# Kernel tuning notes

Hardware: AMD Instinct MI355X
Metric: run time of the kernel (lower is better)

Reference implementation:

```python
import jax, jax.numpy as jnp
import numpy as np

B, S, D, U = 32, 2048, 1024, 1024


def setup_inputs() -> dict:
    key = jax.random.key(0)
    ks = jax.random.split(key, 8)
    scale_in = 1.0 / np.sqrt(D)
    scale_u = 1.0 / np.sqrt(U)
    return {
        "query": jax.random.normal(ks[0], (B, D), dtype=jnp.float32),
        "values": jax.random.normal(ks[1], (B, S, D), dtype=jnp.float32),
        "W1": jax.random.normal(ks[2], (D, U), dtype=jnp.float32) * scale_in,
        "b1": jnp.zeros((U,), dtype=jnp.float32),
        "W2": jax.random.normal(ks[3], (D, U), dtype=jnp.float32) * scale_in,
        "b2": jnp.zeros((U,), dtype=jnp.float32),
        "V": jax.random.normal(ks[4], (U, 1), dtype=jnp.float32) * scale_u,
        "bV": jnp.zeros((1,), dtype=jnp.float32),
    }


def reference(query, values, W1, b1, W2, b2, V, bV):
    # values: [B, S, D] -> [B, S, U]; query: [B, D] -> [B, 1, U]
    proj_v = jnp.einsum("bsd,du->bsu", values, W1) + b1
    proj_q = (query @ W2 + b2)[:, None, :]
    # score: [B, S, 1]
    score = jnp.einsum("bsu,uo->bso", jnp.tanh(proj_v + proj_q), V) + bV
    attention_weights = jax.nn.softmax(score, axis=1)
    # context: [B, D]
    context_vector = jnp.sum(attention_weights * values, axis=1)
    return (context_vector, attention_weights)
```

## Files before the change

### kernel.cpp

```cpp
#include <hip/hip_runtime.h>

#define DEVFN __device__ __forceinline__

typedef __attribute__((ext_vector_type(4))) float f32x4;
typedef __attribute__((ext_vector_type(8))) short short8;
typedef __attribute__((ext_vector_type(4))) unsigned int uint4v;
typedef __attribute__((ext_vector_type(8))) unsigned short ushort8;

constexpr int CB = 32;
constexpr int CS = 2048;
constexpr int CD = 1024;
constexpr int CU = 1024;
constexpr int CM = CB * CS;

DEVFN unsigned f2bf_u(float f) {
    unsigned u = __float_as_uint(f);
    return (u + 0x7FFFu + ((u >> 16) & 1u)) >> 16;
}
DEVFN unsigned f2bf_pack(float lo, float hi) {
    return f2bf_u(lo) | (f2bf_u(hi) << 16);
}
DEVFN short8 cvt8(f32x4 a, f32x4 b) {
    uint4v p;
    p[0] = f2bf_pack(a[0], a[1]);
    p[1] = f2bf_pack(a[2], a[3]);
    p[2] = f2bf_pack(b[0], b[1]);
    p[3] = f2bf_pack(b[2], b[3]);
    return __builtin_bit_cast(short8, p);
}
DEVFN float tanh_fast(float x) {
    float e = exp2f(x * 2.885390081777927f);
    return 1.0f - 2.0f * __builtin_amdgcn_rcpf(e + 1.0f);
}

__global__ void k_bias1(const float* __restrict__ q, const float* __restrict__ W2,
                        float* __restrict__ bpart) {
    int dc = blockIdx.x, b = blockIdx.y;
    int t = threadIdx.x;
    __shared__ float qs[128];
    if (t < 128) qs[t] = q[b * CD + dc * 128 + t];
    __syncthreads();
    float acc0 = 0.f, acc1 = 0.f, acc2 = 0.f, acc3 = 0.f;
    const float* w2 = W2 + (size_t)(dc * 128) * CU + t;
#pragma unroll 4
    for (int d = 0; d < 128; ++d) {
        float qv = qs[d];
        const float* r = w2 + (size_t)d * CU;
        acc0 += qv * r[0];
        acc1 += qv * r[256];
        acc2 += qv * r[512];
        acc3 += qv * r[768];
    }
    float* o = bpart + (size_t)(b * 8 + dc) * CU + t;
    o[0] = acc0; o[256] = acc1; o[512] = acc2; o[768] = acc3;
}

__global__ void k_bias2(const float* __restrict__ bpart, const float* __restrict__ b1,
                        const float* __restrict__ b2, float* __restrict__ bias) {
    int idx = blockIdx.x * 256 + threadIdx.x;
    int b = idx >> 10, u = idx & 1023;
    float s = b1[u] + b2[u];
#pragma unroll
    for (int dc = 0; dc < 8; ++dc) s += bpart[(size_t)(b * 8 + dc) * CU + u];
    bias[idx] = s;
}

__global__ void k_packW1(const float* __restrict__ W1, unsigned short* __restrict__ W1p) {
    int tid = blockIdx.x * 256 + threadIdx.x;
    int o8  = tid * 8;
    int l   = (o8 >> 3) & 63;
    int ub  = (o8 >> 9) & 15;
    int ut  = (o8 >> 13) & 3;
    int kt  = o8 >> 15;
    int u  = ut * 256 + ub * 16 + (l & 15);
    int d0 = kt * 32 + (l >> 4) * 8;
    ushort8 v;
#pragma unroll
    for (int j = 0; j < 8; ++j)
        v[j] = (unsigned short)f2bf_u(W1[(size_t)(d0 + j) * CU + u]);
    *(ushort8*)(W1p + o8) = v;
}

__global__ __launch_bounds__(512, 2) void k_score(
    const float* __restrict__ values, const unsigned short* __restrict__ W1p,
    const float* __restrict__ bias, const float* __restrict__ V,
    float* __restrict__ score2) {
    __shared__ __align__(16) char smem[16384];

    const int t = threadIdx.x;
    const int w = t >> 6, l = t & 63;
    const int p = blockIdx.x;
    const int xt = (p & 7) + (p >> 4) * 8;
    const int uc = (p >> 3) & 1;
    const int ph = (p >> 3) & 31;
    const int m0 = xt * 128;
    const int bb = m0 >> 11;

    const float* aSrcT = values + (size_t)(m0 + (t >> 2)) * CD + (t & 3) * 8;
    const int aWrOff = (t >> 6) * 1024
                     + (((((t >> 2) & 15) ^ (t & 3)) | ((t & 3) << 4)) << 4);
    const int aRdOff = ((((l & 15) ^ (l >> 4)) | ((l >> 4) << 4)) << 4);
    const unsigned short* bBase = W1p + (size_t)(uc * 2 + (w >> 2)) * 8192
                                + (w & 3) * 2048 + l * 8;

    f32x4 acc[8][4];
#pragma unroll
    for (int i = 0; i < 8; ++i)
#pragma unroll
        for (int j = 0; j < 4; ++j) acc[i][j] = f32x4{0.f, 0.f, 0.f, 0.f};

    short8 bF0[4], bF1[4];
    f32x4 s0a, s0b, s1a, s1b;

    {
        const unsigned short* bs = bBase + (size_t)ph * 32768;
#pragma unroll
        for (int jj = 0; jj < 4; ++jj)
            bF0[jj] = *(const short8*)(bs + jj * 512);
        f32x4 ta = __builtin_nontemporal_load((const f32x4*)(aSrcT + ph * 32));
        f32x4 tb = __builtin_nontemporal_load((const f32x4*)(aSrcT + ph * 32 + 4));
        *(short8*)(smem + aWrOff) = cvt8(ta, tb);
        const int kp1 = (ph + 1) & 31;
        s1a = __builtin_nontemporal_load((const f32x4*)(aSrcT + kp1 * 32));
        s1b = __builtin_nontemporal_load((const f32x4*)(aSrcT + kp1 * 32 + 4));
        asm volatile("s_waitcnt lgkmcnt(0)" ::: "memory");
        asm volatile("s_barrier" ::: "memory");
    }

#define SCORE_BODY(KT, BF_CUR, BF_NXT, SLa, SLb, SWa, SWb, DO_LDB, DO_LDA, DO_WR)  \
    {                                                                               \
        if (DO_LDB) {                                                               \
            const int kp = ((KT) + 1 + ph) & 31;                                    \
            const unsigned short* bs = bBase + (size_t)kp * 32768;                  \
            _Pragma("unroll")                                                       \
            for (int jj = 0; jj < 4; ++jj)                                          \
                BF_NXT[jj] = *(const short8*)(bs + jj * 512);                       \
        }                                                                           \
        if (DO_LDA) {                                                               \
            const int kp = ((KT) + 2 + ph) & 31;                                    \
            SLa = __builtin_nontemporal_load((const f32x4*)(aSrcT + kp * 32));      \
            SLb = __builtin_nontemporal_load((const f32x4*)(aSrcT + kp * 32 + 4));  \
        }                                                                           \
        const char* aB = smem + ((KT) & 1) * 8192;                                  \
        short8 aF[8];                                                               \
        _Pragma("unroll")                                                           \
        for (int i = 0; i < 8; ++i)                                                 \
            aF[i] = *(const short8*)(aB + i * 1024 + aRdOff);                       \
        __builtin_amdgcn_s_setprio(1);                                              \
        _Pragma("unroll")                                                           \
        for (int i = 0; i < 8; ++i)                                                 \
            _Pragma("unroll")                                                       \
            for (int j = 0; j < 4; ++j)                                             \
                acc[i][j] = __builtin_amdgcn_mfma_f32_16x16x32_bf16(                \
                    aF[i], BF_CUR[j], acc[i][j], 0, 0, 0);                          \
        __builtin_amdgcn_s_setprio(0);                                              \
        if (DO_WR)                                                                  \
            *(short8*)(smem + (((KT) + 1) & 1) * 8192 + aWrOff) = cvt8(SWa, SWb);   \
        asm volatile("s_waitcnt lgkmcnt(0)" ::: "memory");                          \
        asm volatile("s_barrier" ::: "memory");                                     \
    }

    for (int kt = 0; kt < 30; kt += 2) {
        SCORE_BODY(kt,     bF0, bF1, s0a, s0b, s1a, s1b, 1, 1, 1)
        SCORE_BODY(kt + 1, bF1, bF0, s1a, s1b, s0a, s0b, 1, 1, 1)
    }
    SCORE_BODY(30, bF0, bF1, s0a, s0b, s1a, s1b, 1, 0, 1)
    SCORE_BODY(31, bF1, bF0, s1a, s1b, s0a, s0b, 0, 0, 0)
#undef SCORE_BODY

    float part[8][4];
#pragma unroll
    for (int i = 0; i < 8; ++i)
#pragma unroll
        for (int rr = 0; rr < 4; ++rr) part[i][rr] = 0.f;

#pragma unroll
    for (int j = 0; j < 4; ++j) {
        const int col = uc * 512 + w * 64 + j * 16 + (l & 15);
        const float vv = V[col];
        const float bz = bias[bb * CU + col];
#pragma unroll
        for (int i = 0; i < 8; ++i)
#pragma unroll
            for (int rr = 0; rr < 4; ++rr)
                part[i][rr] += vv * tanh_fast(acc[i][j][rr] + bz);
    }

    float* red = (float*)smem;
#pragma unroll
    for (int i = 0; i < 8; ++i)
#pragma unroll
        for (int rr = 0; rr < 4; ++rr) {
            float v = part[i][rr];
            v += __shfl_xor(v, 1);
            v += __shfl_xor(v, 2);
            v += __shfl_xor(v, 4);
            v += __shfl_xor(v, 8);
            if ((l & 15) == 0)
                red[w * 128 + i * 16 + (l >> 4) * 4 + rr] = v;
        }
    __syncthreads();
    if (t < 128) {
        float sv = 0.f;
#pragma unroll
        for (int ww = 0; ww < 8; ++ww) sv += red[ww * 128 + t];
        score2[(size_t)uc * CM + m0 + t] = sv;
    }
}

__global__ void k_softmax(const float* __restrict__ score2, float* __restrict__ wts) {
    int b = blockIdx.x, t = threadIdx.x;
    int i0 = b * CS + t, i1 = i0 + 1024;
    float s0 = score2[i0] + score2[CM + i0];
    float s1 = score2[i1] + score2[CM + i1];
    __shared__ float red[16];
    int wv = t >> 6, ln = t & 63;
    float m = fmaxf(s0, s1);
#pragma unroll
    for (int o = 32; o >= 1; o >>= 1) m = fmaxf(m, __shfl_xor(m, o));
    if (ln == 0) red[wv] = m;
    __syncthreads();
    float M = red[0];
#pragma unroll
    for (int k = 1; k < 16; ++k) M = fmaxf(M, red[k]);
    float e0 = __expf(s0 - M), e1 = __expf(s1 - M);
    float sm = e0 + e1;
#pragma unroll
    for (int o = 32; o >= 1; o >>= 1) sm += __shfl_xor(sm, o);
    __syncthreads();
    if (ln == 0) red[wv] = sm;
    __syncthreads();
    float T = 0.f;
#pragma unroll
    for (int k = 0; k < 16; ++k) T += red[k];
    float inv = 1.0f / T;
    wts[i0] = e0 * inv;
    wts[i1] = e1 * inv;
}

__global__ void k_ctx_part(const float* __restrict__ values, const float* __restrict__ wts,
                           float* __restrict__ part) {
    int b = blockIdx.y, sc = blockIdx.x;
    int t = threadIdx.x;
    const float* vb = values + ((size_t)b * CS + sc * 64) * CD + t * 4;
    const float* wb = wts + b * CS + sc * 64;
    f32x4 a = {0.f, 0.f, 0.f, 0.f};
#pragma unroll 8
    for (int s = 0; s < 64; ++s) {
        float wgt = wb[s];
        f32x4 v = *(const f32x4*)(vb + (size_t)s * CD);
        a += v * wgt;
    }
    *(f32x4*)(part + (size_t)(b * 32 + sc) * CD + t * 4) = a;
}

__global__ void k_ctx_red(const float* __restrict__ part, float* __restrict__ ctx) {
    int idx = blockIdx.x * 256 + threadIdx.x;
    int b = idx >> 10, d = idx & 1023;
    float s = 0.f;
#pragma unroll 8
    for (int c = 0; c < 32; ++c) s += part[(size_t)(b * 32 + c) * CD + d];
    ctx[idx] = s;
}

extern "C" void kernel_launch(void* const* d_in, const int* in_sizes, int n_in,
                              void* d_out, int out_size, void* d_ws, size_t ws_size,
                              hipStream_t stream) {
    const float* query  = (const float*)d_in[0];
    const float* values = (const float*)d_in[1];
    const float* W1     = (const float*)d_in[2];
    const float* b1     = (const float*)d_in[3];
    const float* W2     = (const float*)d_in[4];
    const float* b2     = (const float*)d_in[5];
    const float* V      = (const float*)d_in[6];

    float* out = (float*)d_out;
    float* ctx = out;
    float* wts = out + 32768;

    char* ws = (char*)d_ws;
    float*          score2 = (float*)ws;
    float*          bias   = (float*)(ws + (1 << 20));
    unsigned short* W1p    = (unsigned short*)(ws + (1 << 20) + (1 << 17));
    float*          part   = (float*)(ws + (1 << 20) + (1 << 17) + (1 << 21));
    float*          bpart  = part;

    k_bias1<<<dim3(8, 32), 256, 0, stream>>>(query, W2, bpart);
    k_bias2<<<128, 256, 0, stream>>>(bpart, b1, b2, bias);
    k_packW1<<<512, 256, 0, stream>>>(W1, W1p);
    k_score<<<1024, 512, 0, stream>>>(values, W1p, bias, V, score2);
    k_softmax<<<32, 1024, 0, stream>>>(score2, wts);
    k_ctx_part<<<dim3(32, 32), 256, 0, stream>>>(values, wts, part);
    k_ctx_red<<<128, 256, 0, stream>>>(part, ctx);
}
```

Baseline: 248.0 us.

## Split score K-step into two ping-pong phases with barriers and sched fences

Each K-step of the score GEMM now runs as two half-phases. Each half loads four A fragments from LDS and issues part of the next B global loads (plus the next A prefetch and LDS write in the second half), then hits a workgroup barrier before its 16 MFMAs. sched_barrier fences pin the order so memory issue and MFMA clusters interleave across waves, in the style of a ping-pong schedule. The cost is an extra barrier per K-step and less freedom for the compiler to schedule.

```diff
diff --git a/kernel.cpp b/kernel.cpp
--- a/kernel.cpp
+++ b/kernel.cpp
@@ -129,35 +129,65 @@
 
 #define SCORE_BODY(KT, BF_CUR, BF_NXT, SLa, SLb, SWa, SWb, DO_LDB, DO_LDA, DO_WR)  \
     {                                                                               \
-        if (DO_LDB) {                                                               \
-            const int kp = ((KT) + 1 + ph) & 31;                                    \
-            const unsigned short* bs = bBase + (size_t)kp * 32768;                  \
+        const char* aB = smem + ((KT) & 1) * 8192;                                  \
+                         \
+        {                                                                           \
+            short8 aF[4];                                                           \
             _Pragma("unroll")                                                       \
-            for (int jj = 0; jj < 4; ++jj)                                          \
-                BF_NXT[jj] = *(const short8*)(bs + jj * 512);                       \
+            for (int i = 0; i < 4; ++i)                                             \
+                aF[i] = *(const short8*)(aB + i * 1024 + aRdOff);                   \
+            if (DO_LDB) {                                                           \
+                const int kp = ((KT) + 1 + ph) & 31;                                \
+                const unsigned short* bs = bBase + (size_t)kp * 32768;              \
+                BF_NXT[0] = *(const short8*)(bs);                                   \
+                BF_NXT[1] = *(const short8*)(bs + 512);                             \
+            }                                                                       \
+            __builtin_amdgcn_sched_barrier(0);                                      \
+            asm volatile("s_barrier" ::: "memory");                                 \
+            __builtin_amdgcn_sched_barrier(0);                                      \
+            __builtin_amdgcn_s_setprio(1);                                          \
+            _Pragma("unroll")                                                       \
+            for (int i = 0; i < 4; ++i)                                             \
+                _Pragma("unroll")                                                   \
+                for (int j = 0; j < 4; ++j)                                         \
+                    acc[i][j] = __builtin_amdgcn_mfma_f32_16x16x32_bf16(            \
+                        aF[i], BF_CUR[j], acc[i][j], 0, 0, 0);                      \
+            __builtin_amdgcn_s_setprio(0);                                          \
+            __builtin_amdgcn_sched_barrier(0);                                      \
         }                                                                           \
-        if (DO_LDA) {                                                               \
-            const int kp = ((KT) + 2 + ph) & 31;                                    \
-            SLa = __builtin_nontemporal_load((const f32x4*)(aSrcT + kp * 32));      \
-            SLb = __builtin_nontemporal_load((const f32x4*)(aSrcT + kp * 32 + 4));  \
+                       \
+        {                                                                           \
+            short8 aF[4];                                                           \
+            _Pragma("unroll")                                                       \
+            for (int i = 0; i < 4; ++i)                                             \
+                aF[i] = *(const short8*)(aB + (i + 4) * 1024 + aRdOff);             \
+            if (DO_LDB) {                                                           \
+                const int kp = ((KT) + 1 + ph) & 31;                                \
+                const unsigned short* bs = bBase + (size_t)kp * 32768;              \
+                BF_NXT[2] = *(const short8*)(bs + 1024);                            \
+                BF_NXT[3] = *(const short8*)(bs + 1536);                            \
+            }                                                                       \
+            if (DO_LDA) {                                                           \
+                const int kp = ((KT) + 2 + ph) & 31;                                \
+                SLa = __builtin_nontemporal_load((const f32x4*)(aSrcT + kp * 32));  \
+                SLb = __builtin_nontemporal_load((const f32x4*)(aSrcT + kp * 32 + 4)); \
+            }                                                                       \
+            if (DO_WR)                                                              \
+                *(short8*)(smem + (((KT) + 1) & 1) * 8192 + aWrOff) = cvt8(SWa, SWb); \
+            asm volatile("s_waitcnt lgkmcnt(0)" ::: "memory");                      \
+            __builtin_amdgcn_sched_barrier(0);                                      \
+            asm volatile("s_barrier" ::: "memory");                                 \
+            __builtin_amdgcn_sched_barrier(0);                                      \
+            __builtin_amdgcn_s_setprio(1);                                          \
+            _Pragma("unroll")                                                       \
+            for (int i = 0; i < 4; ++i)                                             \
+                _Pragma("unroll")                                                   \
+                for (int j = 0; j < 4; ++j)                                         \
+                    acc[i + 4][j] = __builtin_amdgcn_mfma_f32_16x16x32_bf16(        \
+                        aF[i], BF_CUR[j], acc[i + 4][j], 0, 0, 0);                  \
+            __builtin_amdgcn_s_setprio(0);                                          \
+            __builtin_amdgcn_sched_barrier(0);                                      \
         }                                                                           \
-        const char* aB = smem + ((KT) & 1) * 8192;                                  \
-        short8 aF[8];                                                               \
-        _Pragma("unroll")                                                           \
-        for (int i = 0; i < 8; ++i)                                                 \
-            aF[i] = *(const short8*)(aB + i * 1024 + aRdOff);                       \
-        __builtin_amdgcn_s_setprio(1);                                              \
-        _Pragma("unroll")                                                           \
-        for (int i = 0; i < 8; ++i)                                                 \
-            _Pragma("unroll")                                                       \
-            for (int j = 0; j < 4; ++j)                                             \
-                acc[i][j] = __builtin_amdgcn_mfma_f32_16x16x32_bf16(                \
-                    aF[i], BF_CUR[j], acc[i][j], 0, 0, 0);                          \
-        __builtin_amdgcn_s_setprio(0);                                              \
-        if (DO_WR)                                                                  \
-            *(short8*)(smem + (((KT) + 1) & 1) * 8192 + aWrOff) = cvt8(SWa, SWb);   \
-        asm volatile("s_waitcnt lgkmcnt(0)" ::: "memory");                          \
-        asm volatile("s_barrier" ::: "memory");                                     \
     }
 
     for (int kt = 0; kt < 30; kt += 2) {
```

Measured after the change: 243.8 us. Within noise of the previous version (-1.7%).

## Split score GEMM into four U-chunks with XCD-grouped block mapping

Applied to the files above, without the earlier changes.

Each score block now has 256 threads and covers 128 rows by 256 units, so the grid grows to 2048 blocks writing four partial score planes. The softmax sums those four planes. Block indices are remapped so the four U-chunk blocks of one row tile land on the same XCD and can share its L2 copy of the values tile. The LDS swizzle and staging order also change: the next tile's values are written to LDS before the MFMAs instead of after. In exchange, each values tile is read and converted four times instead of twice, and fewer waves are resident per block.

```diff
diff --git a/kernel.cpp b/kernel.cpp
--- a/kernel.cpp
+++ b/kernel.cpp
@@ -81,27 +81,30 @@
     *(ushort8*)(W1p + o8) = v;
 }
 
-__global__ __launch_bounds__(512, 2) void k_score(
+__global__ __launch_bounds__(256, 2) void k_score(
     const float* __restrict__ values, const unsigned short* __restrict__ W1p,
     const float* __restrict__ bias, const float* __restrict__ V,
-    float* __restrict__ score2) {
+    float* __restrict__ score4) {
     __shared__ __align__(16) char smem[16384];
 
     const int t = threadIdx.x;
     const int w = t >> 6, l = t & 63;
     const int p = blockIdx.x;
-    const int xt = (p & 7) + (p >> 4) * 8;
-    const int uc = (p >> 3) & 1;
-    const int ph = (p >> 3) & 31;
+    const int L = (p & 7) * 256 + (p >> 3);
+    const int xt = L >> 2;
+    const int uc = L & 3;
+    const int ph = xt & 31;
     const int m0 = xt * 128;
     const int bb = m0 >> 11;
 
-    const float* aSrcT = values + (size_t)(m0 + (t >> 2)) * CD + (t & 3) * 8;
-    const int aWrOff = (t >> 6) * 1024
-                     + (((((t >> 2) & 15) ^ (t & 3)) | ((t & 3) << 4)) << 4);
-    const int aRdOff = ((((l & 15) ^ (l >> 4)) | ((l >> 4) << 4)) << 4);
-    const unsigned short* bBase = W1p + (size_t)(uc * 2 + (w >> 2)) * 8192
-                                + (w & 3) * 2048 + l * 8;
+    const float* aSrc0 = values + (size_t)(m0 + (t >> 2)) * CD + (t & 3) * 8;
+    const float* aSrc1 = aSrc0 + (size_t)64 * CD;
+    const int hh = t & 3;
+    const int aWr0 = w * 1024 + (((((t >> 2) & 15) ^ (hh << 2)) | (hh << 4)) << 4);
+    const int aWr1 = aWr0 + 4096;
+    const int hR = l >> 4;
+    const int aRdOff = ((((l & 15) ^ (hR << 2)) | (hR << 4)) << 4);
+    const unsigned short* bBase = W1p + (size_t)uc * 8192 + w * 2048 + l * 8;
 
     f32x4 acc[8][4];
 #pragma unroll
@@ -110,26 +113,39 @@
         for (int j = 0; j < 4; ++j) acc[i][j] = f32x4{0.f, 0.f, 0.f, 0.f};
 
     short8 bF0[4], bF1[4];
-    f32x4 s0a, s0b, s1a, s1b;
+    f32x4 a0a, a0b, a1a, a1b;
 
     {
         const unsigned short* bs = bBase + (size_t)ph * 32768;
 #pragma unroll
         for (int jj = 0; jj < 4; ++jj)
             bF0[jj] = *(const short8*)(bs + jj * 512);
-        f32x4 ta = __builtin_nontemporal_load((const f32x4*)(aSrcT + ph * 32));
-        f32x4 tb = __builtin_nontemporal_load((const f32x4*)(aSrcT + ph * 32 + 4));
-        *(short8*)(smem + aWrOff) = cvt8(ta, tb);
+        a0a = __builtin_nontemporal_load((const f32x4*)(aSrc0 + ph * 32));
+        a0b = __builtin_nontemporal_load((const f32x4*)(aSrc0 + ph * 32 + 4));
+        a1a = __builtin_nontemporal_load((const f32x4*)(aSrc1 + ph * 32));
+        a1b = __builtin_nontemporal_load((const f32x4*)(aSrc1 + ph * 32 + 4));
+        *(short8*)(smem + aWr0) = cvt8(a0a, a0b);
+        *(short8*)(smem + aWr1) = cvt8(a1a, a1b);
         const int kp1 = (ph + 1) & 31;
-        s1a = __builtin_nontemporal_load((const f32x4*)(aSrcT + kp1 * 32));
-        s1b = __builtin_nontemporal_load((const f32x4*)(aSrcT + kp1 * 32 + 4));
+        a0a = __builtin_nontemporal_load((const f32x4*)(aSrc0 + kp1 * 32));
+        a0b = __builtin_nontemporal_load((const f32x4*)(aSrc0 + kp1 * 32 + 4));
+        a1a = __builtin_nontemporal_load((const f32x4*)(aSrc1 + kp1 * 32));
+        a1b = __builtin_nontemporal_load((const f32x4*)(aSrc1 + kp1 * 32 + 4));
         asm volatile("s_waitcnt lgkmcnt(0)" ::: "memory");
         asm volatile("s_barrier" ::: "memory");
     }
 
-#define SCORE_BODY(KT, BF_CUR, BF_NXT, SLa, SLb, SWa, SWb, DO_LDB, DO_LDA, DO_WR)  \
+#define SCORE_BODY(KT, BF_CUR, BF_NXT, DO_WRB, DO_LDA)                              \
     {                                                                               \
-        if (DO_LDB) {                                                               \
+        const char* aB = smem + ((KT) & 1) * 8192;                                  \
+        short8 aF[8];                                                               \
+        _Pragma("unroll")                                                           \
+        for (int i = 0; i < 8; ++i)                                                 \
+            aF[i] = *(const short8*)(aB + i * 1024 + aRdOff);                       \
+        if (DO_WRB) {                                                               \
+            char* wB = smem + (((KT) + 1) & 1) * 8192;                              \
+            *(short8*)(wB + aWr0) = cvt8(a0a, a0b);                                 \
+            *(short8*)(wB + aWr1) = cvt8(a1a, a1b);                                 \
             const int kp = ((KT) + 1 + ph) & 31;                                    \
             const unsigned short* bs = bBase + (size_t)kp * 32768;                  \
             _Pragma("unroll")                                                       \
@@ -138,14 +154,11 @@
         }                                                                           \
         if (DO_LDA) {                                                               \
             const int kp = ((KT) + 2 + ph) & 31;                                    \
-            SLa = __builtin_nontemporal_load((const f32x4*)(aSrcT + kp * 32));      \
-            SLb = __builtin_nontemporal_load((const f32x4*)(aSrcT + kp * 32 + 4));  \
+            a0a = __builtin_nontemporal_load((const f32x4*)(aSrc0 + kp * 32));      \
+            a0b = __builtin_nontemporal_load((const f32x4*)(aSrc0 + kp * 32 + 4));  \
+            a1a = __builtin_nontemporal_load((const f32x4*)(aSrc1 + kp * 32));      \
+            a1b = __builtin_nontemporal_load((const f32x4*)(aSrc1 + kp * 32 + 4));  \
         }                                                                           \
-        const char* aB = smem + ((KT) & 1) * 8192;                                  \
-        short8 aF[8];                                                               \
-        _Pragma("unroll")                                                           \
-        for (int i = 0; i < 8; ++i)                                                 \
-            aF[i] = *(const short8*)(aB + i * 1024 + aRdOff);                       \
         __builtin_amdgcn_s_setprio(1);                                              \
         _Pragma("unroll")                                                           \
         for (int i = 0; i < 8; ++i)                                                 \
@@ -154,18 +167,16 @@
                 acc[i][j] = __builtin_amdgcn_mfma_f32_16x16x32_bf16(                \
                     aF[i], BF_CUR[j], acc[i][j], 0, 0, 0);                          \
         __builtin_amdgcn_s_setprio(0);                                              \
-        if (DO_WR)                                                                  \
-            *(short8*)(smem + (((KT) + 1) & 1) * 8192 + aWrOff) = cvt8(SWa, SWb);   \
         asm volatile("s_waitcnt lgkmcnt(0)" ::: "memory");                          \
         asm volatile("s_barrier" ::: "memory");                                     \
     }
 
     for (int kt = 0; kt < 30; kt += 2) {
-        SCORE_BODY(kt,     bF0, bF1, s0a, s0b, s1a, s1b, 1, 1, 1)
-        SCORE_BODY(kt + 1, bF1, bF0, s1a, s1b, s0a, s0b, 1, 1, 1)
-    }
-    SCORE_BODY(30, bF0, bF1, s0a, s0b, s1a, s1b, 1, 0, 1)
-    SCORE_BODY(31, bF1, bF0, s1a, s1b, s0a, s0b, 0, 0, 0)
+        SCORE_BODY(kt,     bF0, bF1, 1, 1)
+        SCORE_BODY(kt + 1, bF1, bF0, 1, 1)
+    }
+    SCORE_BODY(30, bF0, bF1, 1, 0)
+    SCORE_BODY(31, bF1, bF0, 0, 0)
 #undef SCORE_BODY
 
     float part[8][4];
@@ -176,7 +187,7 @@
 
 #pragma unroll
     for (int j = 0; j < 4; ++j) {
-        const int col = uc * 512 + w * 64 + j * 16 + (l & 15);
+        const int col = uc * 256 + w * 64 + j * 16 + (l & 15);
         const float vv = V[col];
         const float bz = bias[bb * CU + col];
 #pragma unroll
@@ -201,18 +212,16 @@
         }
     __syncthreads();
     if (t < 128) {
-        float sv = 0.f;
-#pragma unroll
-        for (int ww = 0; ww < 8; ++ww) sv += red[ww * 128 + t];
-        score2[(size_t)uc * CM + m0 + t] = sv;
-    }
-}
-
-__global__ void k_softmax(const float* __restrict__ score2, float* __restrict__ wts) {
+        float sv = red[t] + red[128 + t] + red[256 + t] + red[384 + t];
+        score4[(size_t)uc * CM + m0 + t] = sv;
+    }
+}
+
+__global__ void k_softmax(const float* __restrict__ score4, float* __restrict__ wts) {
     int b = blockIdx.x, t = threadIdx.x;
     int i0 = b * CS + t, i1 = i0 + 1024;
-    float s0 = score2[i0] + score2[CM + i0];
-    float s1 = score2[i1] + score2[CM + i1];
+    float s0 = score4[i0] + score4[CM + i0] + score4[2 * CM + i0] + score4[3 * CM + i0];
+    float s1 = score4[i1] + score4[CM + i1] + score4[2 * CM + i1] + score4[3 * CM + i1];
     __shared__ float red[16];
     int wv = t >> 6, ln = t & 63;
     float m = fmaxf(s0, s1);
@@ -279,7 +288,7 @@
     float* wts = out + 32768;
 
     char* ws = (char*)d_ws;
-    float*          score2 = (float*)ws;
+    float*          score4 = (float*)ws;
     float*          bias   = (float*)(ws + (1 << 20));
     unsigned short* W1p    = (unsigned short*)(ws + (1 << 20) + (1 << 17));
     float*          part   = (float*)(ws + (1 << 20) + (1 << 17) + (1 << 21));
@@ -288,8 +297,8 @@
     k_bias1<<<dim3(8, 32), 256, 0, stream>>>(query, W2, bpart);
     k_bias2<<<128, 256, 0, stream>>>(bpart, b1, b2, bias);
     k_packW1<<<512, 256, 0, stream>>>(W1, W1p);
-    k_score<<<1024, 512, 0, stream>>>(values, W1p, bias, V, score2);
-    k_softmax<<<32, 1024, 0, stream>>>(score2, wts);
+    k_score<<<2048, 256, 0, stream>>>(values, W1p, bias, V, score4);
+    k_softmax<<<32, 1024, 0, stream>>>(score4, wts);
     k_ctx_part<<<dim3(32, 32), 256, 0, stream>>>(values, wts, part);
     k_ctx_red<<<128, 256, 0, stream>>>(part, ctx);
 }
```

After: 275.5 us. +11.1%, slower.

## Triple-buffer LDS A tiles with single barrier per k-step and new swizzle

Applied to the files above, without the earlier changes.

Expands the A-operand LDS staging from double to triple buffering. The barrier moves to the start of each k-iteration with a partial lgkmcnt wait, so the write of the next tile overlaps other waves' reads and each step has only one sync. The global prefetch distance grows to three steps, nontemporal loads become regular loads, the LDS swizzle pattern changes, and the starting k-phase is derived from the tile index. This costs 8KB more LDS per block, which may affect occupancy, and it adds a final __syncthreads before the reduction reuses LDS.

```diff
diff --git a/kernel.cpp b/kernel.cpp
--- a/kernel.cpp
+++ b/kernel.cpp
@@ -85,21 +85,21 @@
     const float* __restrict__ values, const unsigned short* __restrict__ W1p,
     const float* __restrict__ bias, const float* __restrict__ V,
     float* __restrict__ score2) {
-    __shared__ __align__(16) char smem[16384];
+    __shared__ __align__(16) char smem[24576];
 
     const int t = threadIdx.x;
     const int w = t >> 6, l = t & 63;
     const int p = blockIdx.x;
     const int xt = (p & 7) + (p >> 4) * 8;
     const int uc = (p >> 3) & 1;
-    const int ph = (p >> 3) & 31;
+    const int ph = xt & 31;
     const int m0 = xt * 128;
     const int bb = m0 >> 11;
 
-    const float* aSrcT = values + (size_t)(m0 + (t >> 2)) * CD + (t & 3) * 8;
-    const int aWrOff = (t >> 6) * 1024
-                     + (((((t >> 2) & 15) ^ (t & 3)) | ((t & 3) << 4)) << 4);
-    const int aRdOff = ((((l & 15) ^ (l >> 4)) | ((l >> 4) << 4)) << 4);
+    const float* aSrc = values + (size_t)(m0 + (t >> 2)) * CD + (t & 3) * 8;
+    const int llw = (l >> 2) | ((l & 3) << 4);
+    const int aWr = w * 1024 + ((llw ^ (((llw >> 4) & 3) << 1)) << 4);
+    const int aRd = (l ^ (((l >> 4) & 3) << 1)) << 4;
     const unsigned short* bBase = W1p + (size_t)(uc * 2 + (w >> 2)) * 8192
                                 + (w & 3) * 2048 + l * 8;
 
@@ -110,62 +110,70 @@
         for (int j = 0; j < 4; ++j) acc[i][j] = f32x4{0.f, 0.f, 0.f, 0.f};
 
     short8 bF0[4], bF1[4];
-    f32x4 s0a, s0b, s1a, s1b;
+    f32x4 pXa, pXb, pYa, pYb;
+    char* ldsR = (char*)smem;
+    char* ldsW = (char*)smem + 16384;
 
     {
-        const unsigned short* bs = bBase + (size_t)ph * 32768;
+        const int k0 = ph, k1 = (ph + 1) & 31, k2 = (ph + 2) & 31;
+        const unsigned short* bs = bBase + (size_t)k0 * 32768;
 #pragma unroll
         for (int jj = 0; jj < 4; ++jj)
             bF0[jj] = *(const short8*)(bs + jj * 512);
-        f32x4 ta = __builtin_nontemporal_load((const f32x4*)(aSrcT + ph * 32));
-        f32x4 tb = __builtin_nontemporal_load((const f32x4*)(aSrcT + ph * 32 + 4));
-        *(short8*)(smem + aWrOff) = cvt8(ta, tb);
-        const int kp1 = (ph + 1) & 31;
-        s1a = __builtin_nontemporal_load((const f32x4*)(aSrcT + kp1 * 32));
-        s1b = __builtin_nontemporal_load((const f32x4*)(aSrcT + kp1 * 32 + 4));
+        pXa = *(const f32x4*)(aSrc + k0 * 32);
+        pXb = *(const f32x4*)(aSrc + k0 * 32 + 4);
+        pYa = *(const f32x4*)(aSrc + k1 * 32);
+        pYb = *(const f32x4*)(aSrc + k1 * 32 + 4);
+        *(short8*)(smem + aWr) = cvt8(pXa, pXb);
+        *(short8*)(smem + 8192 + aWr) = cvt8(pYa, pYb);
+        pYa = *(const f32x4*)(aSrc + k2 * 32);
+        pYb = *(const f32x4*)(aSrc + k2 * 32 + 4);
         asm volatile("s_waitcnt lgkmcnt(0)" ::: "memory");
         asm volatile("s_barrier" ::: "memory");
     }
 
-#define SCORE_BODY(KT, BF_CUR, BF_NXT, SLa, SLb, SWa, SWb, DO_LDB, DO_LDA, DO_WR)  \
+#define SCORE_BODY(KT, BFC, BFN, PWa, PWb, PLa, PLb, DO_LDB, DO_LDA, DO_WR)         \
     {                                                                               \
+        asm volatile("s_waitcnt lgkmcnt(1)" ::: "memory");                          \
+        asm volatile("s_barrier" ::: "memory");                                     \
         if (DO_LDB) {                                                               \
             const int kp = ((KT) + 1 + ph) & 31;                                    \
             const unsigned short* bs = bBase + (size_t)kp * 32768;                  \
             _Pragma("unroll")                                                       \
             for (int jj = 0; jj < 4; ++jj)                                          \
-                BF_NXT[jj] = *(const short8*)(bs + jj * 512);                       \
+                BFN[jj] = *(const short8*)(bs + jj * 512);                          \
         }                                                                           \
         if (DO_LDA) {                                                               \
-            const int kp = ((KT) + 2 + ph) & 31;                                    \
-            SLa = __builtin_nontemporal_load((const f32x4*)(aSrcT + kp * 32));      \
-            SLb = __builtin_nontemporal_load((const f32x4*)(aSrcT + kp * 32 + 4));  \
+            const int kp = ((KT) + 3 + ph) & 31;                                    \
+            PLa = *(const f32x4*)(aSrc + kp * 32);                                  \
+            PLb = *(const f32x4*)(aSrc + kp * 32 + 4);                              \
         }                                                                           \
-        const char* aB = smem + ((KT) & 1) * 8192;                                  \
         short8 aF[8];                                                               \
         _Pragma("unroll")                                                           \
         for (int i = 0; i < 8; ++i)                                                 \
-            aF[i] = *(const short8*)(aB + i * 1024 + aRdOff);                       \
+            aF[i] = *(const short8*)(ldsR + i * 1024 + aRd);                        \
         __builtin_amdgcn_s_setprio(1);                                              \
         _Pragma("unroll")                                                           \
         for (int i = 0; i < 8; ++i)                                                 \
             _Pragma("unroll")                                                       \
             for (int j = 0; j < 4; ++j)                                             \
                 acc[i][j] = __builtin_amdgcn_mfma_f32_16x16x32_bf16(                \
-                    aF[i], BF_CUR[j], acc[i][j], 0, 0, 0);                          \
+                    aF[i], BFC[j], acc[i][j], 0, 0, 0);                             \
         __builtin_amdgcn_s_setprio(0);                                              \
         if (DO_WR)                                                                  \
-            *(short8*)(smem + (((KT) + 1) & 1) * 8192 + aWrOff) = cvt8(SWa, SWb);   \
-        asm volatile("s_waitcnt lgkmcnt(0)" ::: "memory");                          \
-        asm volatile("s_barrier" ::: "memory");                                     \
-    }
-
-    for (int kt = 0; kt < 30; kt += 2) {
-        SCORE_BODY(kt,     bF0, bF1, s0a, s0b, s1a, s1b, 1, 1, 1)
-        SCORE_BODY(kt + 1, bF1, bF0, s1a, s1b, s0a, s0b, 1, 1, 1)
-    }
-    SCORE_BODY(30, bF0, bF1, s0a, s0b, s1a, s1b, 1, 0, 1)
-    SCORE_BODY(31, bF1, bF0, s1a, s1b, s0a, s0b, 0, 0, 0)
+            *(short8*)(ldsW + aWr) = cvt8(PWa, PWb);                                \
+        ldsW = ldsR;                                                                \
+        ldsR = (ldsR == (char*)smem + 16384) ? (char*)smem : ldsR + 8192;           \
+    }
+
+    for (int kt = 0; kt < 28; kt += 2) {
+        SCORE_BODY(kt,     bF0, bF1, pYa, pYb, pXa, pXb, 1, 1, 1)
+        SCORE_BODY(kt + 1, bF1, bF0, pXa, pXb, pYa, pYb, 1, 1, 1)
+    }
+    SCORE_BODY(28, bF0, bF1, pYa, pYb, pXa, pXb, 1, 1, 1)
+    SCORE_BODY(29, bF1, bF0, pXa, pXb, pYa, pYb, 1, 0, 1)
+    SCORE_BODY(30, bF0, bF1, pYa, pYb, pXa, pXb, 1, 0, 0)
+    SCORE_BODY(31, bF1, bF0, pXa, pXb, pYa, pYb, 0, 0, 0)
 #undef SCORE_BODY
 
     float part[8][4];
@@ -186,6 +194,7 @@
                 part[i][rr] += vv * tanh_fast(acc[i][j][rr] + bz);
     }
 
+    __syncthreads();
     float* red = (float*)smem;
 #pragma unroll
     for (int i = 0; i < 8; ++i)
```

New measurement: 220.5 us. 1.13x faster.
